# Kernel optimization log

Hardware: AMD Instinct MI355X
Metric: run time of the kernel (lower is better)

The kernel has to match this reference:

```python
import jax, jax.numpy as jnp
import numpy as np

B, Q, C = 16, 2048, 256
SCORE_THRESH = 0.05   # lowered from 0.7 so the mask is non-trivial with 256 classes
NMS_THRESH = 0.7
LABEL_OFFSET = 1e5    # batched_nms trick: offset boxes per class so cross-class IoU ~ 0


def box_cxcywh_to_xyxy(b):
    cx, cy, w, h = jnp.split(b, 4, axis=-1)
    return jnp.concatenate([cx - 0.5 * w, cy - 0.5 * h, cx + 0.5 * w, cy + 0.5 * h], axis=-1)


def pairwise_iou(boxes):
    # boxes: [N,4] xyxy -> iou: [N,N]
    area = jnp.clip(boxes[:, 2] - boxes[:, 0], 0) * jnp.clip(boxes[:, 3] - boxes[:, 1], 0)
    lt = jnp.maximum(boxes[:, None, :2], boxes[None, :, :2])
    rb = jnp.minimum(boxes[:, None, 2:], boxes[None, :, 2:])
    wh = jnp.clip(rb - lt, 0)
    inter = wh[..., 0] * wh[..., 1]
    union = area[:, None] + area[None, :] - inter
    return inter / jnp.maximum(union, 1e-6)


def nms_single(boxes, scores, labels, valid):
    # Emulates torchvision batched_nms with fixed-size (padded) output:
    # returns score-sorted boxes/scores/labels plus a boolean keep mask.
    n = boxes.shape[0]
    boxes_off = boxes + labels.astype(boxes.dtype)[:, None] * LABEL_OFFSET
    order = jnp.argsort(jnp.where(valid, scores, -jnp.inf))[::-1]
    b_off = boxes_off[order]
    s = scores[order]
    l = labels[order]
    v = valid[order]
    iou = pairwise_iou(b_off)  # [N,N], class-offset so only same-class overlap
    idx = jnp.arange(n)

    def step(keep, x):
        row, i = x  # row: iou of box i vs all
        sup = (row > NMS_THRESH) & (idx > i) & keep[i]
        return keep & ~sup, None

    keep, _ = jax.lax.scan(step, v, (iou, idx))
    return boxes[order], s, l, keep & v


def setup_inputs() -> dict:
    key = jax.random.key(0)
    k1, k2, k3 = jax.random.split(key, 3)
    pred_logits = jax.random.normal(k1, (B, Q, C), dtype=jnp.float32)
    pred_boxes = jax.random.uniform(k2, (B, Q, 4), dtype=jnp.float32)
    target_sizes = jax.random.randint(k3, (B, 2), 480, 1333, dtype=jnp.int32)
    return {"pred_logits": pred_logits, "pred_boxes": pred_boxes, "target_sizes": target_sizes}


def reference(pred_logits, pred_boxes, target_sizes):
    prob = jax.nn.softmax(pred_logits, axis=-1)
    cls_prob = prob[..., :-1]            # drop 'no-object' class
    scores = cls_prob.max(axis=-1)       # [B,Q]
    labels = cls_prob.argmax(axis=-1)    # [B,Q]
    boxes = box_cxcywh_to_xyxy(pred_boxes)
    ts = target_sizes.astype(boxes.dtype)
    img_h, img_w = ts[:, 0], ts[:, 1]
    scale = jnp.stack([img_w, img_h, img_w, img_h], axis=1)  # [B,4]
    boxes = boxes * scale[:, None, :]
    valid = scores >= SCORE_THRESH
    out_boxes, out_scores, out_labels, keep = jax.vmap(nms_single)(boxes, scores, labels, valid)
    return out_boxes, out_scores, out_labels, keep
```

## Files before the change

kernel.cpp:

```cpp
#include <hip/hip_runtime.h>
#include <math.h>

#define NB 16
#define BQ 2048
#define NC 256
#define NL 255

typedef unsigned long long u64;
typedef unsigned int u32;
typedef unsigned short u16;
typedef unsigned char u8;

__device__ __forceinline__ u32 ord_f32(float f) {
  u32 b = __float_as_uint(f);
  return (b & 0x80000000u) ? ~b : (b | 0x80000000u);
}

__device__ __forceinline__ u64 shfl_xor_u64(u64 v, int m) {
  int lo = __shfl_xor((int)(u32)v, m, 64);
  int hi = __shfl_xor((int)(u32)(v >> 32), m, 64);
  return ((u64)(u32)hi << 32) | (u32)lo;
}

__global__ __launch_bounds__(256) void score_box_kernel(
    const float* __restrict__ logits,
    const float* __restrict__ pboxes,
    const int* __restrict__ tsz,
    float* __restrict__ out)
{
#pragma clang fp contract(off)
  const int lane = threadIdx.x & 63;
  const int g = lane & 15;
  const int wv = threadIdx.x >> 6;
  const int q = (blockIdx.x * 4 + wv) * 4 + (lane >> 4);
  const float* row = logits + (size_t)q * NC + g * 16;
  const float4 la = *reinterpret_cast<const float4*>(row);
  const float4 lb4 = *reinterpret_cast<const float4*>(row + 4);
  const float4 lc = *reinterpret_cast<const float4*>(row + 8);
  const float4 ld = *reinterpret_cast<const float4*>(row + 12);

  float m = fmaxf(fmaxf(fmaxf(la.x, la.y), fmaxf(la.z, la.w)),
           fmaxf(fmaxf(fmaxf(lb4.x, lb4.y), fmaxf(lb4.z, lb4.w)),
           fmaxf(fmaxf(fmaxf(lc.x, lc.y), fmaxf(lc.z, lc.w)),
                 fmaxf(fmaxf(ld.x, ld.y), fmaxf(ld.z, ld.w)))));
  #pragma unroll
  for (int d = 1; d < 16; d <<= 1) m = fmaxf(m, __shfl_xor(m, d));

  float4 ea, eb, ec, ed;
  ea.x = expf(la.x - m);  ea.y = expf(la.y - m);  ea.z = expf(la.z - m);  ea.w = expf(la.w - m);
  eb.x = expf(lb4.x - m); eb.y = expf(lb4.y - m); eb.z = expf(lb4.z - m); eb.w = expf(lb4.w - m);
  ec.x = expf(lc.x - m);  ec.y = expf(lc.y - m);  ec.z = expf(lc.z - m);  ec.w = expf(lc.w - m);
  ed.x = expf(ld.x - m);  ed.y = expf(ld.y - m);  ed.z = expf(ld.z - m);  ed.w = expf(ld.w - m);

  float s = (((ea.x + ea.y) + (ea.z + ea.w)) + ((eb.x + eb.y) + (eb.z + eb.w)))
          + (((ec.x + ec.y) + (ec.z + ec.w)) + ((ed.x + ed.y) + (ed.z + ed.w)));
  #pragma unroll
  for (int d = 1; d < 16; d <<= 1) s += __shfl_xor(s, d);

  const int c0 = g * 16;
  float bp = ea.x / s; int bc = c0;
  float p;
  p = ea.y / s; if (p > bp) { bp = p; bc = c0 + 1; }
  p = ea.z / s; if (p > bp) { bp = p; bc = c0 + 2; }
  p = ea.w / s; if (p > bp) { bp = p; bc = c0 + 3; }
  p = eb.x / s; if (p > bp) { bp = p; bc = c0 + 4; }
  p = eb.y / s; if (p > bp) { bp = p; bc = c0 + 5; }
  p = eb.z / s; if (p > bp) { bp = p; bc = c0 + 6; }
  p = eb.w / s; if (p > bp) { bp = p; bc = c0 + 7; }
  p = ec.x / s; if (p > bp) { bp = p; bc = c0 + 8; }
  p = ec.y / s; if (p > bp) { bp = p; bc = c0 + 9; }
  p = ec.z / s; if (p > bp) { bp = p; bc = c0 + 10; }
  p = ec.w / s; if (p > bp) { bp = p; bc = c0 + 11; }
  p = ed.x / s; if (p > bp) { bp = p; bc = c0 + 12; }
  p = ed.y / s; if (p > bp) { bp = p; bc = c0 + 13; }
  p = ed.z / s; if (p > bp) { bp = p; bc = c0 + 14; }
  p = ed.w / s; if (g != 15 && p > bp) { bp = p; bc = c0 + 15; }
  #pragma unroll
  for (int d = 1; d < 16; d <<= 1) {
    const float op = __shfl_xor(bp, d);
    const int   oc = __shfl_xor(bc, d);
    if (op > bp || (op == bp && oc < bc)) { bp = op; bc = oc; }
  }

  if (g == 0) {
    const int b = q >> 11;
    float hf = (float)tsz[b * 2 + 0];
    float wf = (float)tsz[b * 2 + 1];
    float4 pb = *reinterpret_cast<const float4*>(pboxes + (size_t)q * 4);
    float hw = 0.5f * pb.z, hh = 0.5f * pb.w;
    float4 ob;
    ob.x = (pb.x - hw) * wf;
    ob.y = (pb.y - hh) * hf;
    ob.z = (pb.x + hw) * wf;
    ob.w = (pb.y + hh) * hf;
    *reinterpret_cast<float4*>(out + (size_t)q * 4) = ob;
    out[NB * BQ * 4 + q] = bp;
    out[NB * BQ * 5 + q] = (float)bc;
  }
}

__global__ __launch_bounds__(1024) void sort_nms_kernel(float* __restrict__ out)
{
#pragma clang fp contract(off)
  __shared__ __align__(16) u64 key[BQ];
  __shared__ float4 bx[BQ];
  __shared__ float sc[BQ];
  __shared__ u8 lb[BQ];
  __shared__ u8 kp[BQ];
  __shared__ u16 gpos[BQ];
  __shared__ u64 ovlg[BQ];
  __shared__ u16 hist[32 * 256];
  __shared__ u32 tot[256];
  __shared__ u32 scn[256];
  __shared__ u32 wval[16], winv[16];

  const int b = blockIdx.x;
  const int tid = threadIdx.x;
  const int lane = tid & 63;
  const int wv = tid >> 6;
  float* boxes_g  = out + (size_t)b * BQ * 4;
  float* scores_g = out + NB * BQ * 4 + (size_t)b * BQ;
  float* labels_g = out + NB * BQ * 5 + (size_t)b * BQ;
  float* keep_g   = out + NB * BQ * 6 + (size_t)b * BQ;

  const int q0 = 2 * tid;
  float2 s2 = *reinterpret_cast<const float2*>(scores_g + q0);
  float2 lf = *reinterpret_cast<const float2*>(labels_g + q0);
  float4 bb0 = *reinterpret_cast<const float4*>(boxes_g + (size_t)q0 * 4);
  float4 bb1 = *reinterpret_cast<const float4*>(boxes_g + (size_t)q0 * 4 + 4);
  sc[q0] = s2.x; sc[q0 + 1] = s2.y;
  lb[q0] = (u8)(int)lf.x; lb[q0 + 1] = (u8)(int)lf.y;
  bx[q0] = bb0; bx[q0 + 1] = bb1;
  const bool v0 = (s2.x >= 0.05f), v1 = (s2.y >= 0.05f);
  u64 f0 = ((u64)(v0 ? ord_f32(s2.x) : 0x007FFFFFu) << 32) | (u32)q0;
  u64 f1 = ((u64)(v1 ? ord_f32(s2.y) : 0x007FFFFFu) << 32) | (u32)(q0 + 1);
  const u64 b0 = __ballot(v0), b1 = __ballot(v1);
  if (lane == 0) {
    const u32 c = (u32)(__popcll(b0) + __popcll(b1));
    wval[wv] = c;
    winv[wv] = 128u - c;
  }
  __syncthreads();

  int nv = 0, voff = 0, ioff = 0;
  #pragma unroll
  for (int w = 0; w < 16; ++w) {
    const int c = (int)wval[w];
    nv += c;
    if (w < wv) { voff += c; ioff += (int)winv[w]; }
  }
  const int tinv = BQ - nv;
  const u64 below = (1ull << lane) - 1ull;
  const int vr0 = voff + (int)__popcll(b0 & below) + (int)__popcll(b1 & below);
  const int ir0 = ioff + (int)__popcll(~b0 & below) + (int)__popcll(~b1 & below);
  const int vr1 = vr0 + (v0 ? 1 : 0);
  const int ir1 = ir0 + (v0 ? 0 : 1);
  const int ip0 = v0 ? vr0 : (nv + (tinv - 1 - ir0));
  const int ip1 = v1 ? vr1 : (nv + (tinv - 1 - ir1));

  {
    ulonglong2 z; z.x = 0; z.y = 0;
    *reinterpret_cast<ulonglong2*>(&key[q0]) = z;
  }
  __syncthreads();
  if (v0) key[ip0] = f0;
  if (v1) key[ip1] = f1;
  __syncthreads();

  u32 P = 1;
  while ((int)P < nv) P <<= 1;
  const bool wactive = ((u32)(q0 & ~127) < P);

  u64 e0 = key[q0], e1 = key[q0 + 1];
  for (u32 k = 2; k <= P; k <<= 1) {
    for (u32 j = k >> 1; j > 0; j >>= 1) {
      const bool up = (((u32)q0 & k) == 0);
      if (j >= 128) {
        if (wactive) {
          ulonglong2 w2; w2.x = e0; w2.y = e1;
          *reinterpret_cast<ulonglong2*>(&key[q0]) = w2;
        }
        __syncthreads();
        if (wactive) {
          const u32 pb = (u32)q0 ^ j;
          ulonglong2 part = *reinterpret_cast<const ulonglong2*>(&key[pb]);
          const bool keepmax = ((((u32)q0 & j) == 0) == up);
          e0 = keepmax ? (e0 > part.x ? e0 : part.x) : (e0 < part.x ? e0 : part.x);
          e1 = keepmax ? (e1 > part.y ? e1 : part.y) : (e1 < part.y ? e1 : part.y);
        }
        __syncthreads();
      } else if (wactive) {
        if (j >= 2) {
          const int j2 = (int)(j >> 1);
          const u64 y0 = shfl_xor_u64(e0, j2);
          const u64 y1 = shfl_xor_u64(e1, j2);
          const bool keepmax = (((lane & j2) == 0) == up);
          e0 = keepmax ? (e0 > y0 ? e0 : y0) : (e0 < y0 ? e0 : y0);
          e1 = keepmax ? (e1 > y1 ? e1 : y1) : (e1 < y1 ? e1 : y1);
        } else {
          const u64 mx = e0 > e1 ? e0 : e1;
          const u64 mn = e0 > e1 ? e1 : e0;
          e0 = up ? mx : mn;
          e1 = up ? mn : mx;
        }
      }
    }
  }
  if (wactive) {
    ulonglong2 w2; w2.x = e0; w2.y = e1;
    *reinterpret_cast<ulonglong2*>(&key[q0]) = w2;
  }
  __syncthreads();

  if (!v0) key[ip0] = f0;
  if (!v1) key[ip1] = f1;
  kp[tid] = 0; kp[tid + 1024] = 0;
  reinterpret_cast<u32*>(hist)[tid]        = 0;
  reinterpret_cast<u32*>(hist)[tid + 1024] = 0;
  reinterpret_cast<u32*>(hist)[tid + 2048] = 0;
  reinterpret_cast<u32*>(hist)[tid + 3072] = 0;
  __syncthreads();

  int lA, lB; u32 rA, rB;
  {
    const int p = tid;
    const u32 oi = (u32)key[p] & (BQ - 1);
    lA = (p < nv) ? (int)lb[oi] : 255;
    u64 m = ~0ull;
    #pragma unroll
    for (int bt = 0; bt < 8; ++bt) {
      const u64 vb = __ballot(((lA >> bt) & 1));
      m &= ((lA >> bt) & 1) ? vb : ~vb;
    }
    rA = (u32)__popcll(m & below);
    if (lane == 63 - __builtin_clzll(m)) hist[(p >> 6) * 256 + lA] = (u16)__popcll(m);
  }
  {
    const int p = tid + 1024;
    const u32 oi = (u32)key[p] & (BQ - 1);
    lB = (p < nv) ? (int)lb[oi] : 255;
    u64 m = ~0ull;
    #pragma unroll
    for (int bt = 0; bt < 8; ++bt) {
      const u64 vb = __ballot(((lB >> bt) & 1));
      m &= ((lB >> bt) & 1) ? vb : ~vb;
    }
    rB = (u32)__popcll(m & below);
    if (lane == 63 - __builtin_clzll(m)) hist[(p >> 6) * 256 + lB] = (u16)__popcll(m);
  }
  __syncthreads();

  if (tid < 256) {
    u32 run = 0;
    #pragma unroll
    for (int c = 0; c < 32; ++c) {
      const u32 v = hist[c * 256 + tid];
      hist[c * 256 + tid] = (u16)run;
      run += v;
    }
    tot[tid] = run;
  }
  __syncthreads();

  if (tid < 64) {
    u32 carry = 0;
    for (int seg = 0; seg < 4; ++seg) {
      const int l = seg * 64 + tid;
      u32 x = tot[l];
      #pragma unroll
      for (int s = 1; s < 64; s <<= 1) {
        const u32 y = __shfl_up(x, s, 64);
        if (lane >= s) x += y;
      }
      scn[l] = x + carry;
      carry += __shfl(x, 63, 64);
    }
  }
  __syncthreads();

  u32 gA, gB;
  {
    const int p = tid;
    const u32 st = (lA == 0) ? 0u : scn[lA - 1];
    gA = (u32)hist[(p >> 6) * 256 + lA] + rA;
    gpos[st + gA] = (u16)p;
  }
  {
    const int p = tid + 1024;
    const u32 st = (lB == 0) ? 0u : scn[lB - 1];
    gB = (u32)hist[(p >> 6) * 256 + lB] + rB;
    gpos[st + gB] = (u16)p;
  }
  __syncthreads();

  #pragma unroll
  for (int half = 0; half < 2; ++half) {
    const int p = tid + half * 1024;
    const int l = half ? lB : lA;
    const u32 g = half ? gB : gA;
    if (p < nv && g < 64) {
      const u32 st = (l == 0) ? 0u : scn[l - 1];
      const u32 oi = (u32)key[p] & (BQ - 1);
      const float4 A = bx[oi];
      const float lc = (float)l * 100000.0f;
      const float ax1 = A.x + lc, ay1 = A.y + lc, ax2 = A.z + lc, ay2 = A.w + lc;
      const float areaA = fmaxf(ax2 - ax1, 0.0f) * fmaxf(ay2 - ay1, 0.0f);
      u64 m = 0;
      for (u32 r = 0; r < g; ++r) {
        const int p2 = gpos[st + r];
        const u32 oj = (u32)key[p2] & (BQ - 1);
        const float4 Bb = bx[oj];
        const float bx1 = Bb.x + lc, by1 = Bb.y + lc, bx2 = Bb.z + lc, by2 = Bb.w + lc;
        const float areaB = fmaxf(bx2 - bx1, 0.0f) * fmaxf(by2 - by1, 0.0f);
        const float ltx = fmaxf(ax1, bx1), lty = fmaxf(ay1, by1);
        const float rbx = fminf(ax2, bx2), rby = fminf(ay2, by2);
        const float iw = fmaxf(rbx - ltx, 0.0f), ih = fmaxf(rby - lty, 0.0f);
        const float inter = iw * ih;
        const float uni = (areaA + areaB) - inter;
        const float iou = inter / fmaxf(uni, 1e-6f);
        if (iou > 0.7f) m |= (1ull << r);
      }
      ovlg[st + g] = m;
    }
  }
  __syncthreads();

  if (tid < NL) {
    const int l = tid;
    const int st = (l == 0) ? 0 : (int)scn[l - 1];
    const int en = (int)scn[l];
    const int k = en - st;
    if (k <= 64) {
      u64 kept = 0;
      for (int r = 0; r < k; ++r) {
        const u64 m = ovlg[st + r];
        const int keep = ((m & kept) == 0) ? 1 : 0;
        kept |= (u64)keep << r;
        kp[gpos[st + r]] = (u8)keep;
      }
    } else {
      const float lc = (float)l * 100000.0f;
      for (int a = st; a < en; ++a) {
        const int p = gpos[a];
        const u32 oi = (u32)key[p] & (BQ - 1);
        const float4 A = bx[oi];
        const float ax1 = A.x + lc, ay1 = A.y + lc, ax2 = A.z + lc, ay2 = A.w + lc;
        const float areaA = fmaxf(ax2 - ax1, 0.0f) * fmaxf(ay2 - ay1, 0.0f);
        int keep = 1;
        for (int e = st; e < a; ++e) {
          const int q2 = gpos[e];
          if (!kp[q2]) continue;
          const u32 oj = (u32)key[q2] & (BQ - 1);
          const float4 Bb = bx[oj];
          const float bx1 = Bb.x + lc, by1 = Bb.y + lc, bx2 = Bb.z + lc, by2 = Bb.w + lc;
          const float areaB = fmaxf(bx2 - bx1, 0.0f) * fmaxf(by2 - by1, 0.0f);
          const float ltx = fmaxf(ax1, bx1), lty = fmaxf(ay1, by1);
          const float rbx = fminf(ax2, bx2), rby = fminf(ay2, by2);
          const float iw = fmaxf(rbx - ltx, 0.0f), ih = fmaxf(rby - lty, 0.0f);
          const float inter = iw * ih;
          const float uni = (areaA + areaB) - inter;
          const float iou = inter / fmaxf(uni, 1e-6f);
          if (iou > 0.7f) { keep = 0; break; }
        }
        kp[p] = (u8)keep;
      }
    }
  }
  __syncthreads();

  {
    const int p = tid;
    const u32 oi = (u32)key[p] & (BQ - 1);
    *reinterpret_cast<float4*>(boxes_g + (size_t)p * 4) = bx[oi];
    scores_g[p] = sc[oi];
    labels_g[p] = (float)lb[oi];
    keep_g[p]   = kp[p] ? 1.0f : 0.0f;
  }
  {
    const int p = tid + 1024;
    const u32 oi = (u32)key[p] & (BQ - 1);
    *reinterpret_cast<float4*>(boxes_g + (size_t)p * 4) = bx[oi];
    scores_g[p] = sc[oi];
    labels_g[p] = (float)lb[oi];
    keep_g[p]   = kp[p] ? 1.0f : 0.0f;
  }
}

extern "C" void kernel_launch(void* const* d_in, const int* in_sizes, int n_in,
                              void* d_out, int out_size, void* d_ws, size_t ws_size,
                              hipStream_t stream) {
  const float* logits = (const float*)d_in[0];
  const float* pboxes = (const float*)d_in[1];
  const int*   tsz    = (const int*)d_in[2];
  float* out = (float*)d_out;
  score_box_kernel<<<NB * BQ / 16, 256, 0, stream>>>(logits, pboxes, tsz, out);
  sort_nms_kernel<<<NB, 1024, 0, stream>>>(out);
}
```

Baseline: 33.57 us.

## Replace bitonic sort and label histogram with fused rank-counting sort

Swaps the shared-memory bitonic sort and the separate per-label histogram/scan pass for one rank-counting pass. Each valid key is compared against all other valid keys, which gives its global sorted position, its rank within its class and its class start offset in a single loop. Labels are packed into the key and class-offset boxes are precomputed once so the IoU loops skip the recomputation. This removes many barrier-separated sort and scan phases, but costs O(nv^2) comparisons that grow with the number of valid boxes.

```diff
diff --git a/kernel.cpp b/kernel.cpp
--- a/kernel.cpp
+++ b/kernel.cpp
@@ -14,12 +14,6 @@
 __device__ __forceinline__ u32 ord_f32(float f) {
   u32 b = __float_as_uint(f);
   return (b & 0x80000000u) ? ~b : (b | 0x80000000u);
-}
-
-__device__ __forceinline__ u64 shfl_xor_u64(u64 v, int m) {
-  int lo = __shfl_xor((int)(u32)v, m, 64);
-  int hi = __shfl_xor((int)(u32)(v >> 32), m, 64);
-  return ((u64)(u32)hi << 32) | (u32)lo;
 }
 
 __global__ __launch_bounds__(256) void score_box_kernel(
@@ -103,15 +97,16 @@
 {
 #pragma clang fp contract(off)
   __shared__ __align__(16) u64 key[BQ];
+  __shared__ __align__(16) u64 ovlg[BQ];
   __shared__ float4 bx[BQ];
+  __shared__ float4 bxo[BQ];
   __shared__ float sc[BQ];
   __shared__ u8 lb[BQ];
   __shared__ u8 kp[BQ];
+  __shared__ u16 gof[BQ];
   __shared__ u16 gpos[BQ];
-  __shared__ u64 ovlg[BQ];
-  __shared__ u16 hist[32 * 256];
-  __shared__ u32 tot[256];
-  __shared__ u32 scn[256];
+  __shared__ u32 offl[256];
+  __shared__ u32 kcnt[256];
   __shared__ u32 wval[16], winv[16];
 
   const int b = blockIdx.x;
@@ -129,17 +124,19 @@
   float4 bb0 = *reinterpret_cast<const float4*>(boxes_g + (size_t)q0 * 4);
   float4 bb1 = *reinterpret_cast<const float4*>(boxes_g + (size_t)q0 * 4 + 4);
   sc[q0] = s2.x; sc[q0 + 1] = s2.y;
-  lb[q0] = (u8)(int)lf.x; lb[q0 + 1] = (u8)(int)lf.y;
+  const u32 l0 = (u32)(int)lf.x, l1 = (u32)(int)lf.y;
+  lb[q0] = (u8)l0; lb[q0 + 1] = (u8)l1;
   bx[q0] = bb0; bx[q0 + 1] = bb1;
   const bool v0 = (s2.x >= 0.05f), v1 = (s2.y >= 0.05f);
-  u64 f0 = ((u64)(v0 ? ord_f32(s2.x) : 0x007FFFFFu) << 32) | (u32)q0;
-  u64 f1 = ((u64)(v1 ? ord_f32(s2.y) : 0x007FFFFFu) << 32) | (u32)(q0 + 1);
+  const u64 f0 = ((u64)(v0 ? ord_f32(s2.x) : 0x007FFFFFu) << 32) | ((u32)q0 << 8) | l0;
+  const u64 f1 = ((u64)(v1 ? ord_f32(s2.y) : 0x007FFFFFu) << 32) | ((u32)(q0 + 1) << 8) | l1;
   const u64 b0 = __ballot(v0), b1 = __ballot(v1);
   if (lane == 0) {
     const u32 c = (u32)(__popcll(b0) + __popcll(b1));
     wval[wv] = c;
     winv[wv] = 128u - c;
   }
+  if (tid < 256) kcnt[tid] = 0;
   __syncthreads();
 
   int nv = 0, voff = 0, ioff = 0;
@@ -155,214 +152,117 @@
   const int ir0 = ioff + (int)__popcll(~b0 & below) + (int)__popcll(~b1 & below);
   const int vr1 = vr0 + (v0 ? 1 : 0);
   const int ir1 = ir0 + (v0 ? 0 : 1);
-  const int ip0 = v0 ? vr0 : (nv + (tinv - 1 - ir0));
-  const int ip1 = v1 ? vr1 : (nv + (tinv - 1 - ir1));
-
-  {
-    ulonglong2 z; z.x = 0; z.y = 0;
-    *reinterpret_cast<ulonglong2*>(&key[q0]) = z;
-  }
-  __syncthreads();
-  if (v0) key[ip0] = f0;
-  if (v1) key[ip1] = f1;
-  __syncthreads();
-
-  u32 P = 1;
-  while ((int)P < nv) P <<= 1;
-  const bool wactive = ((u32)(q0 & ~127) < P);
-
-  u64 e0 = key[q0], e1 = key[q0 + 1];
-  for (u32 k = 2; k <= P; k <<= 1) {
-    for (u32 j = k >> 1; j > 0; j >>= 1) {
-      const bool up = (((u32)q0 & k) == 0);
-      if (j >= 128) {
-        if (wactive) {
-          ulonglong2 w2; w2.x = e0; w2.y = e1;
-          *reinterpret_cast<ulonglong2*>(&key[q0]) = w2;
-        }
-        __syncthreads();
-        if (wactive) {
-          const u32 pb = (u32)q0 ^ j;
-          ulonglong2 part = *reinterpret_cast<const ulonglong2*>(&key[pb]);
-          const bool keepmax = ((((u32)q0 & j) == 0) == up);
-          e0 = keepmax ? (e0 > part.x ? e0 : part.x) : (e0 < part.x ? e0 : part.x);
-          e1 = keepmax ? (e1 > part.y ? e1 : part.y) : (e1 < part.y ? e1 : part.y);
-        }
-        __syncthreads();
-      } else if (wactive) {
-        if (j >= 2) {
-          const int j2 = (int)(j >> 1);
-          const u64 y0 = shfl_xor_u64(e0, j2);
-          const u64 y1 = shfl_xor_u64(e1, j2);
-          const bool keepmax = (((lane & j2) == 0) == up);
-          e0 = keepmax ? (e0 > y0 ? e0 : y0) : (e0 < y0 ? e0 : y0);
-          e1 = keepmax ? (e1 > y1 ? e1 : y1) : (e1 < y1 ? e1 : y1);
-        } else {
-          const u64 mx = e0 > e1 ? e0 : e1;
-          const u64 mn = e0 > e1 ? e1 : e0;
-          e0 = up ? mx : mn;
-          e1 = up ? mn : mx;
-        }
+  if (v0) ovlg[vr0] = f0; else { const int ip = nv + (tinv - 1 - ir0); key[ip] = f0; kp[ip] = 0; }
+  if (v1) ovlg[vr1] = f1; else { const int ip = nv + (tinv - 1 - ir1); key[ip] = f1; kp[ip] = 0; }
+  __syncthreads();
+
+  if (nv > 0) {
+    u32 S = 1; int logS = 0;
+    while ((int)S < nv) { S <<= 1; ++logS; }
+    int tshift = 10 - logS; if (tshift < 0) tshift = 0; if (tshift > 6) tshift = 6;
+    const int tps = 1 << tshift;
+    const int qtr = tid & (tps - 1);
+    const int sstep = 1024 >> tshift;
+    for (int slot = tid >> tshift; slot < nv; slot += sstep) {
+      const u64 ki = ovlg[slot];
+      const u32 li = (u32)ki & 255u;
+      const int jlo = (nv * qtr) >> tshift;
+      const int jhi = (nv * (qtr + 1)) >> tshift;
+      int cgt = 0, lgt = 0, llt = 0;
+      for (int j = jlo; j < jhi; ++j) {
+        const u64 kj = ovlg[j];
+        const u32 lj = (u32)kj & 255u;
+        cgt += (kj > ki) ? 1 : 0;
+        lgt += ((kj > ki) & (lj == li)) ? 1 : 0;
+        llt += (lj < li) ? 1 : 0;
+      }
+      #pragma unroll
+      for (int d = 1; d < 64; d <<= 1) {
+        if (d >= tps) break;
+        cgt += __shfl_xor(cgt, d);
+        lgt += __shfl_xor(lgt, d);
+        llt += __shfl_xor(llt, d);
+      }
+      if (qtr == 0) {
+        const int p = cgt;
+        key[p] = ki;
+        gof[p] = (u16)lgt;
+        gpos[llt + lgt] = (u16)p;
+        offl[li] = (u32)llt;
+        atomicAdd(&kcnt[li], 1u);
+        const u32 oi = (u32)(ki >> 8) & (BQ - 1);
+        const float lc = (float)li * 100000.0f;
+        const float4 A = bx[oi];
+        float4 Ao;
+        Ao.x = A.x + lc; Ao.y = A.y + lc; Ao.z = A.z + lc; Ao.w = A.w + lc;
+        bxo[p] = Ao;
       }
     }
-  }
-  if (wactive) {
-    ulonglong2 w2; w2.x = e0; w2.y = e1;
-    *reinterpret_cast<ulonglong2*>(&key[q0]) = w2;
-  }
-  __syncthreads();
-
-  if (!v0) key[ip0] = f0;
-  if (!v1) key[ip1] = f1;
-  kp[tid] = 0; kp[tid + 1024] = 0;
-  reinterpret_cast<u32*>(hist)[tid]        = 0;
-  reinterpret_cast<u32*>(hist)[tid + 1024] = 0;
-  reinterpret_cast<u32*>(hist)[tid + 2048] = 0;
-  reinterpret_cast<u32*>(hist)[tid + 3072] = 0;
-  __syncthreads();
-
-  int lA, lB; u32 rA, rB;
-  {
-    const int p = tid;
-    const u32 oi = (u32)key[p] & (BQ - 1);
-    lA = (p < nv) ? (int)lb[oi] : 255;
-    u64 m = ~0ull;
-    #pragma unroll
-    for (int bt = 0; bt < 8; ++bt) {
-      const u64 vb = __ballot(((lA >> bt) & 1));
-      m &= ((lA >> bt) & 1) ? vb : ~vb;
-    }
-    rA = (u32)__popcll(m & below);
-    if (lane == 63 - __builtin_clzll(m)) hist[(p >> 6) * 256 + lA] = (u16)__popcll(m);
-  }
-  {
-    const int p = tid + 1024;
-    const u32 oi = (u32)key[p] & (BQ - 1);
-    lB = (p < nv) ? (int)lb[oi] : 255;
-    u64 m = ~0ull;
-    #pragma unroll
-    for (int bt = 0; bt < 8; ++bt) {
-      const u64 vb = __ballot(((lB >> bt) & 1));
-      m &= ((lB >> bt) & 1) ? vb : ~vb;
-    }
-    rB = (u32)__popcll(m & below);
-    if (lane == 63 - __builtin_clzll(m)) hist[(p >> 6) * 256 + lB] = (u16)__popcll(m);
-  }
-  __syncthreads();
-
-  if (tid < 256) {
-    u32 run = 0;
-    #pragma unroll
-    for (int c = 0; c < 32; ++c) {
-      const u32 v = hist[c * 256 + tid];
-      hist[c * 256 + tid] = (u16)run;
-      run += v;
-    }
-    tot[tid] = run;
-  }
-  __syncthreads();
-
-  if (tid < 64) {
-    u32 carry = 0;
-    for (int seg = 0; seg < 4; ++seg) {
-      const int l = seg * 64 + tid;
-      u32 x = tot[l];
-      #pragma unroll
-      for (int s = 1; s < 64; s <<= 1) {
-        const u32 y = __shfl_up(x, s, 64);
-        if (lane >= s) x += y;
-      }
-      scn[l] = x + carry;
-      carry += __shfl(x, 63, 64);
-    }
-  }
-  __syncthreads();
-
-  u32 gA, gB;
-  {
-    const int p = tid;
-    const u32 st = (lA == 0) ? 0u : scn[lA - 1];
-    gA = (u32)hist[(p >> 6) * 256 + lA] + rA;
-    gpos[st + gA] = (u16)p;
-  }
-  {
-    const int p = tid + 1024;
-    const u32 st = (lB == 0) ? 0u : scn[lB - 1];
-    gB = (u32)hist[(p >> 6) * 256 + lB] + rB;
-    gpos[st + gB] = (u16)p;
   }
   __syncthreads();
 
   #pragma unroll
   for (int half = 0; half < 2; ++half) {
     const int p = tid + half * 1024;
-    const int l = half ? lB : lA;
-    const u32 g = half ? gB : gA;
-    if (p < nv && g < 64) {
-      const u32 st = (l == 0) ? 0u : scn[l - 1];
-      const u32 oi = (u32)key[p] & (BQ - 1);
-      const float4 A = bx[oi];
-      const float lc = (float)l * 100000.0f;
-      const float ax1 = A.x + lc, ay1 = A.y + lc, ax2 = A.z + lc, ay2 = A.w + lc;
-      const float areaA = fmaxf(ax2 - ax1, 0.0f) * fmaxf(ay2 - ay1, 0.0f);
-      u64 m = 0;
-      for (u32 r = 0; r < g; ++r) {
-        const int p2 = gpos[st + r];
-        const u32 oj = (u32)key[p2] & (BQ - 1);
-        const float4 Bb = bx[oj];
-        const float bx1 = Bb.x + lc, by1 = Bb.y + lc, bx2 = Bb.z + lc, by2 = Bb.w + lc;
-        const float areaB = fmaxf(bx2 - bx1, 0.0f) * fmaxf(by2 - by1, 0.0f);
-        const float ltx = fmaxf(ax1, bx1), lty = fmaxf(ay1, by1);
-        const float rbx = fminf(ax2, bx2), rby = fminf(ay2, by2);
-        const float iw = fmaxf(rbx - ltx, 0.0f), ih = fmaxf(rby - lty, 0.0f);
-        const float inter = iw * ih;
-        const float uni = (areaA + areaB) - inter;
-        const float iou = inter / fmaxf(uni, 1e-6f);
-        if (iou > 0.7f) m |= (1ull << r);
-      }
-      ovlg[st + g] = m;
-    }
-  }
-  __syncthreads();
-
-  if (tid < NL) {
-    const int l = tid;
-    const int st = (l == 0) ? 0 : (int)scn[l - 1];
-    const int en = (int)scn[l];
-    const int k = en - st;
-    if (k <= 64) {
-      u64 kept = 0;
-      for (int r = 0; r < k; ++r) {
-        const u64 m = ovlg[st + r];
-        const int keep = ((m & kept) == 0) ? 1 : 0;
-        kept |= (u64)keep << r;
-        kp[gpos[st + r]] = (u8)keep;
-      }
-    } else {
-      const float lc = (float)l * 100000.0f;
-      for (int a = st; a < en; ++a) {
-        const int p = gpos[a];
-        const u32 oi = (u32)key[p] & (BQ - 1);
-        const float4 A = bx[oi];
-        const float ax1 = A.x + lc, ay1 = A.y + lc, ax2 = A.z + lc, ay2 = A.w + lc;
-        const float areaA = fmaxf(ax2 - ax1, 0.0f) * fmaxf(ay2 - ay1, 0.0f);
-        int keep = 1;
-        for (int e = st; e < a; ++e) {
-          const int q2 = gpos[e];
-          if (!kp[q2]) continue;
-          const u32 oj = (u32)key[q2] & (BQ - 1);
-          const float4 Bb = bx[oj];
-          const float bx1 = Bb.x + lc, by1 = Bb.y + lc, bx2 = Bb.z + lc, by2 = Bb.w + lc;
-          const float areaB = fmaxf(bx2 - bx1, 0.0f) * fmaxf(by2 - by1, 0.0f);
-          const float ltx = fmaxf(ax1, bx1), lty = fmaxf(ay1, by1);
-          const float rbx = fminf(ax2, bx2), rby = fminf(ay2, by2);
+    if (p < nv) {
+      const u32 li = (u32)key[p] & 255u;
+      const u32 g = gof[p];
+      if (g < 64) {
+        const u32 st = offl[li];
+        const float4 Ao = bxo[p];
+        const float areaA = fmaxf(Ao.z - Ao.x, 0.0f) * fmaxf(Ao.w - Ao.y, 0.0f);
+        u64 m = 0;
+        for (u32 r = 0; r < g; ++r) {
+          const int p2 = gpos[st + r];
+          const float4 Bo = bxo[p2];
+          const float areaB = fmaxf(Bo.z - Bo.x, 0.0f) * fmaxf(Bo.w - Bo.y, 0.0f);
+          const float ltx = fmaxf(Ao.x, Bo.x), lty = fmaxf(Ao.y, Bo.y);
+          const float rbx = fminf(Ao.z, Bo.z), rby = fminf(Ao.w, Bo.w);
           const float iw = fmaxf(rbx - ltx, 0.0f), ih = fmaxf(rby - lty, 0.0f);
           const float inter = iw * ih;
           const float uni = (areaA + areaB) - inter;
           const float iou = inter / fmaxf(uni, 1e-6f);
-          if (iou > 0.7f) { keep = 0; break; }
+          if (iou > 0.7f) m |= (1ull << r);
         }
-        kp[p] = (u8)keep;
+        ovlg[st + g] = m;
+      }
+    }
+  }
+  __syncthreads();
+
+  if (tid < NL) {
+    const int k = (int)kcnt[tid];
+    if (k > 0) {
+      const int st = (int)offl[tid];
+      if (k <= 64) {
+        u64 kept = 0;
+        for (int r = 0; r < k; ++r) {
+          const u64 m = ovlg[st + r];
+          const int keep = ((m & kept) == 0) ? 1 : 0;
+          kept |= (u64)keep << r;
+          kp[gpos[st + r]] = (u8)keep;
+        }
+      } else {
+        for (int a = 0; a < k; ++a) {
+          const int p = gpos[st + a];
+          const float4 Ao = bxo[p];
+          const float areaA = fmaxf(Ao.z - Ao.x, 0.0f) * fmaxf(Ao.w - Ao.y, 0.0f);
+          int keep = 1;
+          for (int e = 0; e < a; ++e) {
+            const int p2 = gpos[st + e];
+            if (!kp[p2]) continue;
+            const float4 Bo = bxo[p2];
+            const float areaB = fmaxf(Bo.z - Bo.x, 0.0f) * fmaxf(Bo.w - Bo.y, 0.0f);
+            const float ltx = fmaxf(Ao.x, Bo.x), lty = fmaxf(Ao.y, Bo.y);
+            const float rbx = fminf(Ao.z, Bo.z), rby = fminf(Ao.w, Bo.w);
+            const float iw = fmaxf(rbx - ltx, 0.0f), ih = fmaxf(rby - lty, 0.0f);
+            const float inter = iw * ih;
+            const float uni = (areaA + areaB) - inter;
+            const float iou = inter / fmaxf(uni, 1e-6f);
+            if (iou > 0.7f) { keep = 0; break; }
+          }
+          kp[p] = (u8)keep;
+        }
       }
     }
   }
@@ -370,7 +270,7 @@
 
   {
     const int p = tid;
-    const u32 oi = (u32)key[p] & (BQ - 1);
+    const u32 oi = (u32)(key[p] >> 8) & (BQ - 1);
     *reinterpret_cast<float4*>(boxes_g + (size_t)p * 4) = bx[oi];
     scores_g[p] = sc[oi];
     labels_g[p] = (float)lb[oi];
@@ -378,7 +278,7 @@
   }
   {
     const int p = tid + 1024;
-    const u32 oi = (u32)key[p] & (BQ - 1);
+    const u32 oi = (u32)(key[p] >> 8) & (BQ - 1);
     *reinterpret_cast<float4*>(boxes_g + (size_t)p * 4) = bx[oi];
     scores_g[p] = sc[oi];
     labels_g[p] = (float)lb[oi];
```

After: 54.22 us. 1.62x slower.
